# Kernel optimization log

Measured on AMD Instinct MI355X. Metric: run time of the kernel, lower is better.

The kernel has to match this reference:

```python
import jax, jax.numpy as jnp
import numpy as np

DIM = 64
HEADS = 4
SHAPE = (2, 64, 64, 64, DIM)  # [n, h, w, d, C] channels-last


def setup_inputs() -> dict:
    key = jax.random.key(0)
    ks = jax.random.split(key, 9)
    s = 1.0 / np.sqrt(DIM)
    return {
        "x": jax.random.normal(ks[0], SHAPE, dtype=jnp.float32),
        "Wk": jax.random.normal(ks[1], (DIM, DIM), dtype=jnp.float32) * s,
        "bk": jax.random.normal(ks[2], (DIM,), dtype=jnp.float32) * 0.01,
        "Wq": jax.random.normal(ks[3], (DIM, DIM), dtype=jnp.float32) * s,
        "bq": jax.random.normal(ks[4], (DIM,), dtype=jnp.float32) * 0.01,
        "Wv": jax.random.normal(ks[5], (DIM, DIM), dtype=jnp.float32) * s,
        "bv": jax.random.normal(ks[6], (DIM,), dtype=jnp.float32) * 0.01,
        "Wr": jax.random.normal(ks[7], (DIM, DIM), dtype=jnp.float32) * s,
        "br": jax.random.normal(ks[8], (DIM,), dtype=jnp.float32) * 0.01,
        "head_count": HEADS,
    }


def reference(x, Wk, bk, Wq, bq, Wv, bv, Wr, br, head_count):
    n, h, w, d, C = x.shape
    N = h * w * d
    H = head_count
    dk = C // H  # head key channels == head value channels (key/value channels = dim)

    xf = x.reshape(n, N, C)  # tokens along flattened spatial axis
    # Conv3d with 1x1x1 kernel == per-token linear projection over channels
    k = xf @ Wk.T + bk  # [n, N, C]
    q = xf @ Wq.T + bq
    v = xf @ Wv.T + bv

    # split channels into contiguous head chunks -> [n, H, dk, N]
    k = k.reshape(n, N, H, dk).transpose(0, 2, 3, 1)
    q = q.reshape(n, N, H, dk).transpose(0, 2, 3, 1)
    v = v.reshape(n, N, H, dk).transpose(0, 2, 3, 1)

    k = jax.nn.softmax(k, axis=3)  # softmax over spatial positions
    q = jax.nn.softmax(q, axis=2)  # softmax over head key channels

    # context = softmax(K) @ V^T : [n, H, dk, dv]
    ctx = jnp.einsum('nhkN,nhvN->nhkv', k, v)
    # attended = context^T @ softmax(Q) : [n, H, dv, N]
    att = jnp.einsum('nhkv,nhkN->nhvN', ctx, q)

    agg = att.transpose(0, 3, 1, 2).reshape(n, N, C)  # concat heads on channels
    out = agg @ Wr.T + br  # reprojection (1x1x1 conv)
    return out.reshape(n, h, w, d, C)
```

## Files before the change

kernel.cpp:

```cpp
#include <hip/hip_runtime.h>
#include <math.h>


#define NTOK 262144
typedef float4 f4;
typedef _Float16 f16;
typedef __attribute__((ext_vector_type(8))) _Float16 f16x8;
typedef __attribute__((ext_vector_type(4))) _Float16 f16x4;
typedef __attribute__((ext_vector_type(4))) float f32x4;

#define WS_S  0
#define WS_Z  2048
#define WS_MH 2176

__device__ __forceinline__ f16x8 cvt8h2(f4 a, f4 b) {
    f16x8 r;
    r[0] = (f16)a.x; r[1] = (f16)a.y; r[2] = (f16)a.z; r[3] = (f16)a.w;
    r[4] = (f16)b.x; r[5] = (f16)b.y; r[6] = (f16)b.z; r[7] = (f16)b.w;
    return r;
}

__global__ __launch_bounds__(256) void k_init(float* __restrict__ ws) {
    int i = blockIdx.x * 256 + threadIdx.x;
    if (i < 2176) ws[i] = 0.0f;
}

__global__ __launch_bounds__(256) void k_ctx(const float* __restrict__ x,
                                             const float* __restrict__ Wk,
                                             const float* __restrict__ Wv,
                                             float* __restrict__ ws) {
    __shared__ float sr[4096];
    __shared__ float zr[256];

    const int tid  = threadIdx.x;
    const int w    = tid >> 6;
    const int lane = tid & 63;
    const int lr   = lane & 15;
    const int ql   = lane >> 4;

    const int nb = blockIdx.x >> 9;
    const int bi = blockIdx.x & 511;
    const long base = (long)nb * NTOK + (long)bi * 512 + (long)w * 128;

    f16x8 wkf[4][2], wvf[4][2];
    #pragma unroll
    for (int h = 0; h < 4; ++h) {
        const float* kr = &Wk[(16 * h + lr) * 64 + 8 * ql];
        const float* vr = &Wv[(16 * h + lr) * 64 + 8 * ql];
        #pragma unroll
        for (int jc = 0; jc < 2; ++jc) {
            wkf[h][jc] = cvt8h2(*(const f4*)&kr[32 * jc], *(const f4*)&kr[32 * jc + 4]);
            wvf[h][jc] = cvt8h2(*(const f4*)&vr[32 * jc], *(const f4*)&vr[32 * jc + 4]);
        }
    }

    const f32x4 zero4 = {0.f, 0.f, 0.f, 0.f};
    f32x4 S[4] = {zero4, zero4, zero4, zero4};
    float z[4] = {0.f, 0.f, 0.f, 0.f};

    f4 A0, A1, A2, A3, B0, B1, B2, B3;
    {
        const float* xp = x + (((size_t)(base + lr)) << 6) + 8 * ql;
        A0 = *(const f4*)xp;        A1 = *(const f4*)(xp + 4);
        A2 = *(const f4*)(xp + 32); A3 = *(const f4*)(xp + 36);
        const float* yp = x + (((size_t)(base + 16 + lr)) << 6) + 8 * ql;
        B0 = *(const f4*)yp;        B1 = *(const f4*)(yp + 4);
        B2 = *(const f4*)(yp + 32); B3 = *(const f4*)(yp + 36);
    }

    for (int s = 0; s < 4; ++s) {
        {
            f16x8 a0 = cvt8h2(A0, A1), a1 = cvt8h2(A2, A3);
            if (s < 3) {
                const float* xp = x + (((size_t)(base + (2 * s + 2) * 16 + lr)) << 6) + 8 * ql;
                A0 = *(const f4*)xp;        A1 = *(const f4*)(xp + 4);
                A2 = *(const f4*)(xp + 32); A3 = *(const f4*)(xp + 36);
            }
            #pragma unroll
            for (int h = 0; h < 4; ++h) {
                f32x4 ak = zero4, av = zero4;
                ak = __builtin_amdgcn_mfma_f32_16x16x32_f16(a0, wkf[h][0], ak, 0, 0, 0);
                ak = __builtin_amdgcn_mfma_f32_16x16x32_f16(a1, wkf[h][1], ak, 0, 0, 0);
                av = __builtin_amdgcn_mfma_f32_16x16x32_f16(a0, wvf[h][0], av, 0, 0, 0);
                av = __builtin_amdgcn_mfma_f32_16x16x32_f16(a1, wvf[h][1], av, 0, 0, 0);
                const float e0 = __expf(ak[0]), e1 = __expf(ak[1]);
                const float e2 = __expf(ak[2]), e3 = __expf(ak[3]);
                z[h] += (e0 + e1) + (e2 + e3);
                f16x4 ekf = {(f16)e0, (f16)e1, (f16)e2, (f16)e3};
                f16x4 evf = {(f16)av[0], (f16)av[1], (f16)av[2], (f16)av[3]};
                S[h] = __builtin_amdgcn_mfma_f32_16x16x16f16(ekf, evf, S[h], 0, 0, 0);
            }
        }
        {
            f16x8 a0 = cvt8h2(B0, B1), a1 = cvt8h2(B2, B3);
            if (s < 3) {
                const float* xp = x + (((size_t)(base + (2 * s + 3) * 16 + lr)) << 6) + 8 * ql;
                B0 = *(const f4*)xp;        B1 = *(const f4*)(xp + 4);
                B2 = *(const f4*)(xp + 32); B3 = *(const f4*)(xp + 36);
            }
            #pragma unroll
            for (int h = 0; h < 4; ++h) {
                f32x4 ak = zero4, av = zero4;
                ak = __builtin_amdgcn_mfma_f32_16x16x32_f16(a0, wkf[h][0], ak, 0, 0, 0);
                ak = __builtin_amdgcn_mfma_f32_16x16x32_f16(a1, wkf[h][1], ak, 0, 0, 0);
                av = __builtin_amdgcn_mfma_f32_16x16x32_f16(a0, wvf[h][0], av, 0, 0, 0);
                av = __builtin_amdgcn_mfma_f32_16x16x32_f16(a1, wvf[h][1], av, 0, 0, 0);
                const float e0 = __expf(ak[0]), e1 = __expf(ak[1]);
                const float e2 = __expf(ak[2]), e3 = __expf(ak[3]);
                z[h] += (e0 + e1) + (e2 + e3);
                f16x4 ekf = {(f16)e0, (f16)e1, (f16)e2, (f16)e3};
                f16x4 evf = {(f16)av[0], (f16)av[1], (f16)av[2], (f16)av[3]};
                S[h] = __builtin_amdgcn_mfma_f32_16x16x16f16(ekf, evf, S[h], 0, 0, 0);
            }
        }
    }

    #pragma unroll
    for (int h = 0; h < 4; ++h) {
        z[h] += __shfl_xor(z[h], 16);
        z[h] += __shfl_xor(z[h], 32);
    }

    #pragma unroll
    for (int h = 0; h < 4; ++h) {
        #pragma unroll
        for (int r = 0; r < 4; ++r)
            sr[((w * 4 + h) * 16 + 4 * ql + r) * 16 + lr] = S[h][r];
        if (lane < 16) zr[(w * 4 + h) * 16 + lane] = z[h];
    }
    __syncthreads();
    #pragma unroll
    for (int i = 0; i < 4; ++i) {
        const int idx = i * 256 + tid;
        const float acc = sr[idx] + sr[1024 + idx] + sr[2048 + idx] + sr[3072 + idx];
        atomicAdd(&ws[WS_S + nb * 1024 + idx], acc);
    }
    if (tid < 64) {
        const float acc = zr[tid] + zr[64 + tid] + zr[128 + tid] + zr[192 + tid];
        atomicAdd(&ws[WS_Z + nb * 64 + tid], acc);
    }
}

__global__ __launch_bounds__(256) void k_m(const float* __restrict__ Wr,
                                           const float* __restrict__ bv,
                                           float* __restrict__ ws) {
    const int n = blockIdx.x >> 4;
    const int i = (blockIdx.x & 15) * 256 + threadIdx.x;
    f16* MH = (f16*)(ws + WS_MH);
    const int c = i >> 6, p = i & 63;
    const int h = p >> 4, kc = p & 15;
    const float rz = 1.0f / ws[WS_Z + n * 64 + p];
    const float* Srow = ws + WS_S + n * 1024 + h * 256 + kc * 16;
    const float* Wrow = Wr + c * 64 + h * 16;
    const float* bvr  = bv + h * 16;
    float acc = 0.f, accb = 0.f;
    #pragma unroll
    for (int vc = 0; vc < 16; ++vc) {
        acc  += Wrow[vc] * Srow[vc];
        accb += Wrow[vc] * bvr[vc];
    }
    MH[n * 4096 + c * 64 + p] = (f16)(acc * rz + accb);
}

__global__ __launch_bounds__(256) void k_out(const float* __restrict__ x,
                                             const float* __restrict__ Wq,
                                             const float* __restrict__ bq,
                                             const float* __restrict__ br,
                                             float* __restrict__ out,
                                             const float* __restrict__ ws) {
    const int tid  = threadIdx.x;
    const int w    = tid >> 6;
    const int lane = tid & 63;
    const int lr   = lane & 15;
    const int ql   = lane >> 4;

    const int nb = blockIdx.x >> 10;
    const int bi = blockIdx.x & 1023;
    const long base = (long)nb * NTOK + (long)bi * 256 + (long)w * 64;

    f16x8 wqf[4][2];
    f16x4 bqh[4];
    #pragma unroll
    for (int h = 0; h < 4; ++h) {
        const float* qr = &Wq[(16 * h + lr) * 64 + 8 * ql];
        #pragma unroll
        for (int jc = 0; jc < 2; ++jc)
            wqf[h][jc] = cvt8h2(*(const f4*)&qr[32 * jc], *(const f4*)&qr[32 * jc + 4]);
        const f4 b = *(const f4*)&bq[16 * h + 4 * ql];
        bqh[h][0] = (f16)b.x; bqh[h][1] = (f16)b.y;
        bqh[h][2] = (f16)b.z; bqh[h][3] = (f16)b.w;
    }
    f16x4 mfa[4][4];
    f16x4 brh[4];
    const f16* MH = (const f16*)(ws + WS_MH) + (size_t)nb * 4096;
    #pragma unroll
    for (int oct = 0; oct < 4; ++oct) {
        #pragma unroll
        for (int pc = 0; pc < 4; ++pc)
            mfa[oct][pc] = *(const f16x4*)&MH[(16 * oct + lr) * 64 + 16 * pc + 4 * ql];
        const f4 b = *(const f4*)&br[16 * oct + 4 * ql];
        brh[oct][0] = (f16)b.x; brh[oct][1] = (f16)b.y;
        brh[oct][2] = (f16)b.z; brh[oct][3] = (f16)b.w;
    }

    const f32x4 zero4 = {0.f, 0.f, 0.f, 0.f};

    f4 L0, L1, L2, L3;
    {
        const float* xp = x + (((size_t)(base + lr)) << 6) + 8 * ql;
        L0 = *(const f4*)xp;        L1 = *(const f4*)(xp + 4);
        L2 = *(const f4*)(xp + 32); L3 = *(const f4*)(xp + 36);
    }

    for (int s = 0; s < 4; ++s) {
        f16x8 b0 = cvt8h2(L0, L1), b1 = cvt8h2(L2, L3);
        if (s < 3) {
            const float* xp = x + (((size_t)(base + (s + 1) * 16 + lr)) << 6) + 8 * ql;
            L0 = *(const f4*)xp;        L1 = *(const f4*)(xp + 4);
            L2 = *(const f4*)(xp + 32); L3 = *(const f4*)(xp + 36);
        }
        f16x4 qf[4];
        #pragma unroll
        for (int h = 0; h < 4; ++h) {
            f32x4 aq = zero4;
            aq = __builtin_amdgcn_mfma_f32_16x16x32_f16(wqf[h][0], b0, aq, 0, 0, 0);
            aq = __builtin_amdgcn_mfma_f32_16x16x32_f16(wqf[h][1], b1, aq, 0, 0, 0);
            float q0 = aq[0] + (float)bqh[h][0], q1 = aq[1] + (float)bqh[h][1];
            float q2 = aq[2] + (float)bqh[h][2], q3 = aq[3] + (float)bqh[h][3];
            float mx = fmaxf(fmaxf(q0, q1), fmaxf(q2, q3));
            mx = fmaxf(mx, __shfl_xor(mx, 16));
            mx = fmaxf(mx, __shfl_xor(mx, 32));
            float e0 = __expf(q0 - mx), e1 = __expf(q1 - mx);
            float e2 = __expf(q2 - mx), e3 = __expf(q3 - mx);
            float sm = (e0 + e1) + (e2 + e3);
            sm += __shfl_xor(sm, 16);
            sm += __shfl_xor(sm, 32);
            const float rs = 1.0f / sm;
            qf[h][0] = (f16)(e0 * rs); qf[h][1] = (f16)(e1 * rs);
            qf[h][2] = (f16)(e2 * rs); qf[h][3] = (f16)(e3 * rs);
        }
        const size_t obase = ((size_t)(base + s * 16 + lr)) << 6;
        #pragma unroll
        for (int oct = 0; oct < 4; ++oct) {
            f32x4 o = zero4;
            #pragma unroll
            for (int pc = 0; pc < 4; ++pc)
                o = __builtin_amdgcn_mfma_f32_16x16x16f16(mfa[oct][pc], qf[pc], o, 0, 0, 0);
            const f4 res = {o[0] + (float)brh[oct][0], o[1] + (float)brh[oct][1],
                            o[2] + (float)brh[oct][2], o[3] + (float)brh[oct][3]};
            *(f4*)&out[obase + 16 * oct + 4 * ql] = res;
        }
    }
}

extern "C" void kernel_launch(void* const* d_in, const int* in_sizes, int n_in,
                              void* d_out, int out_size, void* d_ws, size_t ws_size,
                              hipStream_t stream) {
    const float* x  = (const float*)d_in[0];
    const float* Wk = (const float*)d_in[1];
    const float* Wq = (const float*)d_in[3];
    const float* bq = (const float*)d_in[4];
    const float* Wv = (const float*)d_in[5];
    const float* bv = (const float*)d_in[6];
    const float* Wr = (const float*)d_in[7];
    const float* br = (const float*)d_in[8];
    float* out = (float*)d_out;
    float* ws  = (float*)d_ws;

    hipLaunchKernelGGL(k_init, dim3(9),    dim3(256), 0, stream, ws);
    hipLaunchKernelGGL(k_ctx,  dim3(1024), dim3(256), 0, stream, x, Wk, Wv, ws);
    hipLaunchKernelGGL(k_m,    dim3(32),   dim3(256), 0, stream, Wr, bv, ws);
    hipLaunchKernelGGL(k_out,  dim3(2048), dim3(256), 0, stream, x, Wq, bq, br, out, ws);
}
```

Baseline: 127.4 us.

## Split context reduction across more blocks with 16 partial-sum slots

The context kernel now launches four times as many blocks, each covering 128 tokens (32 per wave, with no inner loop), to raise parallelism and occupancy. Atomic accumulation is spread over 16 partial buffers per batch, selected by block index, to reduce contention on the same addresses. The small M kernel then sums the 16 partial S and Z slices. In exchange, the per-block cost of loading and converting the weights is paid over less work, there are more atomics overall, and the init kernel must zero a larger buffer.

```diff
diff --git a/kernel.cpp b/kernel.cpp
--- a/kernel.cpp
+++ b/kernel.cpp
@@ -9,9 +9,9 @@
 typedef __attribute__((ext_vector_type(4))) _Float16 f16x4;
 typedef __attribute__((ext_vector_type(4))) float f32x4;
 
-#define WS_S  0
-#define WS_Z  2048
 #define WS_MH 2176
+#define WS_SP 6272
+#define WS_ZP 39040
 
 __device__ __forceinline__ f16x8 cvt8h2(f4 a, f4 b) {
     f16x8 r;
@@ -22,7 +22,7 @@
 
 __global__ __launch_bounds__(256) void k_init(float* __restrict__ ws) {
     int i = blockIdx.x * 256 + threadIdx.x;
-    if (i < 2176) ws[i] = 0.0f;
+    if (i < 34816) ws[WS_SP + i] = 0.0f;
 }
 
 __global__ __launch_bounds__(256) void k_ctx(const float* __restrict__ x,
@@ -38,25 +38,10 @@
     const int lr   = lane & 15;
     const int ql   = lane >> 4;
 
-    const int nb = blockIdx.x >> 9;
-    const int bi = blockIdx.x & 511;
-    const long base = (long)nb * NTOK + (long)bi * 512 + (long)w * 128;
-
-    f16x8 wkf[4][2], wvf[4][2];
-    #pragma unroll
-    for (int h = 0; h < 4; ++h) {
-        const float* kr = &Wk[(16 * h + lr) * 64 + 8 * ql];
-        const float* vr = &Wv[(16 * h + lr) * 64 + 8 * ql];
-        #pragma unroll
-        for (int jc = 0; jc < 2; ++jc) {
-            wkf[h][jc] = cvt8h2(*(const f4*)&kr[32 * jc], *(const f4*)&kr[32 * jc + 4]);
-            wvf[h][jc] = cvt8h2(*(const f4*)&vr[32 * jc], *(const f4*)&vr[32 * jc + 4]);
-        }
-    }
-
-    const f32x4 zero4 = {0.f, 0.f, 0.f, 0.f};
-    f32x4 S[4] = {zero4, zero4, zero4, zero4};
-    float z[4] = {0.f, 0.f, 0.f, 0.f};
+    const int nb = blockIdx.x >> 11;
+    const int bi = blockIdx.x & 2047;
+    const int sl = bi & 15;
+    const long base = (long)nb * NTOK + (long)bi * 128 + (long)w * 32;
 
     f4 A0, A1, A2, A3, B0, B1, B2, B3;
     {
@@ -68,50 +53,54 @@
         B2 = *(const f4*)(yp + 32); B3 = *(const f4*)(yp + 36);
     }
 
-    for (int s = 0; s < 4; ++s) {
-        {
-            f16x8 a0 = cvt8h2(A0, A1), a1 = cvt8h2(A2, A3);
-            if (s < 3) {
-                const float* xp = x + (((size_t)(base + (2 * s + 2) * 16 + lr)) << 6) + 8 * ql;
-                A0 = *(const f4*)xp;        A1 = *(const f4*)(xp + 4);
-                A2 = *(const f4*)(xp + 32); A3 = *(const f4*)(xp + 36);
-            }
-            #pragma unroll
-            for (int h = 0; h < 4; ++h) {
-                f32x4 ak = zero4, av = zero4;
-                ak = __builtin_amdgcn_mfma_f32_16x16x32_f16(a0, wkf[h][0], ak, 0, 0, 0);
-                ak = __builtin_amdgcn_mfma_f32_16x16x32_f16(a1, wkf[h][1], ak, 0, 0, 0);
-                av = __builtin_amdgcn_mfma_f32_16x16x32_f16(a0, wvf[h][0], av, 0, 0, 0);
-                av = __builtin_amdgcn_mfma_f32_16x16x32_f16(a1, wvf[h][1], av, 0, 0, 0);
-                const float e0 = __expf(ak[0]), e1 = __expf(ak[1]);
-                const float e2 = __expf(ak[2]), e3 = __expf(ak[3]);
-                z[h] += (e0 + e1) + (e2 + e3);
-                f16x4 ekf = {(f16)e0, (f16)e1, (f16)e2, (f16)e3};
-                f16x4 evf = {(f16)av[0], (f16)av[1], (f16)av[2], (f16)av[3]};
-                S[h] = __builtin_amdgcn_mfma_f32_16x16x16f16(ekf, evf, S[h], 0, 0, 0);
-            }
-        }
-        {
-            f16x8 a0 = cvt8h2(B0, B1), a1 = cvt8h2(B2, B3);
-            if (s < 3) {
-                const float* xp = x + (((size_t)(base + (2 * s + 3) * 16 + lr)) << 6) + 8 * ql;
-                B0 = *(const f4*)xp;        B1 = *(const f4*)(xp + 4);
-                B2 = *(const f4*)(xp + 32); B3 = *(const f4*)(xp + 36);
-            }
-            #pragma unroll
-            for (int h = 0; h < 4; ++h) {
-                f32x4 ak = zero4, av = zero4;
-                ak = __builtin_amdgcn_mfma_f32_16x16x32_f16(a0, wkf[h][0], ak, 0, 0, 0);
-                ak = __builtin_amdgcn_mfma_f32_16x16x32_f16(a1, wkf[h][1], ak, 0, 0, 0);
-                av = __builtin_amdgcn_mfma_f32_16x16x32_f16(a0, wvf[h][0], av, 0, 0, 0);
-                av = __builtin_amdgcn_mfma_f32_16x16x32_f16(a1, wvf[h][1], av, 0, 0, 0);
-                const float e0 = __expf(ak[0]), e1 = __expf(ak[1]);
-                const float e2 = __expf(ak[2]), e3 = __expf(ak[3]);
-                z[h] += (e0 + e1) + (e2 + e3);
-                f16x4 ekf = {(f16)e0, (f16)e1, (f16)e2, (f16)e3};
-                f16x4 evf = {(f16)av[0], (f16)av[1], (f16)av[2], (f16)av[3]};
-                S[h] = __builtin_amdgcn_mfma_f32_16x16x16f16(ekf, evf, S[h], 0, 0, 0);
-            }
+    f16x8 wkf[4][2], wvf[4][2];
+    #pragma unroll
+    for (int h = 0; h < 4; ++h) {
+        const float* kr = &Wk[(16 * h + lr) * 64 + 8 * ql];
+        const float* vr = &Wv[(16 * h + lr) * 64 + 8 * ql];
+        #pragma unroll
+        for (int jc = 0; jc < 2; ++jc) {
+            wkf[h][jc] = cvt8h2(*(const f4*)&kr[32 * jc], *(const f4*)&kr[32 * jc + 4]);
+            wvf[h][jc] = cvt8h2(*(const f4*)&vr[32 * jc], *(const f4*)&vr[32 * jc + 4]);
+        }
+    }
+
+    const f32x4 zero4 = {0.f, 0.f, 0.f, 0.f};
+    f32x4 S[4] = {zero4, zero4, zero4, zero4};
+    float z[4] = {0.f, 0.f, 0.f, 0.f};
+
+    {
+        f16x8 a0 = cvt8h2(A0, A1), a1 = cvt8h2(A2, A3);
+        #pragma unroll
+        for (int h = 0; h < 4; ++h) {
+            f32x4 ak = zero4, av = zero4;
+            ak = __builtin_amdgcn_mfma_f32_16x16x32_f16(a0, wkf[h][0], ak, 0, 0, 0);
+            ak = __builtin_amdgcn_mfma_f32_16x16x32_f16(a1, wkf[h][1], ak, 0, 0, 0);
+            av = __builtin_amdgcn_mfma_f32_16x16x32_f16(a0, wvf[h][0], av, 0, 0, 0);
+            av = __builtin_amdgcn_mfma_f32_16x16x32_f16(a1, wvf[h][1], av, 0, 0, 0);
+            const float e0 = __expf(ak[0]), e1 = __expf(ak[1]);
+            const float e2 = __expf(ak[2]), e3 = __expf(ak[3]);
+            z[h] += (e0 + e1) + (e2 + e3);
+            f16x4 ekf = {(f16)e0, (f16)e1, (f16)e2, (f16)e3};
+            f16x4 evf = {(f16)av[0], (f16)av[1], (f16)av[2], (f16)av[3]};
+            S[h] = __builtin_amdgcn_mfma_f32_16x16x16f16(ekf, evf, S[h], 0, 0, 0);
+        }
+    }
+    {
+        f16x8 a0 = cvt8h2(B0, B1), a1 = cvt8h2(B2, B3);
+        #pragma unroll
+        for (int h = 0; h < 4; ++h) {
+            f32x4 ak = zero4, av = zero4;
+            ak = __builtin_amdgcn_mfma_f32_16x16x32_f16(a0, wkf[h][0], ak, 0, 0, 0);
+            ak = __builtin_amdgcn_mfma_f32_16x16x32_f16(a1, wkf[h][1], ak, 0, 0, 0);
+            av = __builtin_amdgcn_mfma_f32_16x16x32_f16(a0, wvf[h][0], av, 0, 0, 0);
+            av = __builtin_amdgcn_mfma_f32_16x16x32_f16(a1, wvf[h][1], av, 0, 0, 0);
+            const float e0 = __expf(ak[0]), e1 = __expf(ak[1]);
+            const float e2 = __expf(ak[2]), e3 = __expf(ak[3]);
+            z[h] += (e0 + e1) + (e2 + e3);
+            f16x4 ekf = {(f16)e0, (f16)e1, (f16)e2, (f16)e3};
+            f16x4 evf = {(f16)av[0], (f16)av[1], (f16)av[2], (f16)av[3]};
+            S[h] = __builtin_amdgcn_mfma_f32_16x16x16f16(ekf, evf, S[h], 0, 0, 0);
         }
     }
 
@@ -129,15 +118,16 @@
         if (lane < 16) zr[(w * 4 + h) * 16 + lane] = z[h];
     }
     __syncthreads();
+    const int sbase = WS_SP + (sl * 2 + nb) * 1024;
     #pragma unroll
     for (int i = 0; i < 4; ++i) {
         const int idx = i * 256 + tid;
         const float acc = sr[idx] + sr[1024 + idx] + sr[2048 + idx] + sr[3072 + idx];
-        atomicAdd(&ws[WS_S + nb * 1024 + idx], acc);
+        atomicAdd(&ws[sbase + idx], acc);
     }
     if (tid < 64) {
         const float acc = zr[tid] + zr[64 + tid] + zr[128 + tid] + zr[192 + tid];
-        atomicAdd(&ws[WS_Z + nb * 64 + tid], acc);
+        atomicAdd(&ws[WS_ZP + (sl * 2 + nb) * 64 + tid], acc);
     }
 }
 
@@ -149,15 +139,20 @@
     f16* MH = (f16*)(ws + WS_MH);
     const int c = i >> 6, p = i & 63;
     const int h = p >> 4, kc = p & 15;
-    const float rz = 1.0f / ws[WS_Z + n * 64 + p];
-    const float* Srow = ws + WS_S + n * 1024 + h * 256 + kc * 16;
+    float zsum = 0.f;
+    #pragma unroll
+    for (int sl = 0; sl < 16; ++sl)
+        zsum += ws[WS_ZP + (sl * 2 + n) * 64 + p];
+    const float rz = 1.0f / zsum;
     const float* Wrow = Wr + c * 64 + h * 16;
     const float* bvr  = bv + h * 16;
     float acc = 0.f, accb = 0.f;
     #pragma unroll
-    for (int vc = 0; vc < 16; ++vc) {
-        acc  += Wrow[vc] * Srow[vc];
-        accb += Wrow[vc] * bvr[vc];
+    for (int vc = 0; vc < 16; ++vc) accb += Wrow[vc] * bvr[vc];
+    for (int sl = 0; sl < 16; ++sl) {
+        const float* Srow = ws + WS_SP + (sl * 2 + n) * 1024 + h * 256 + kc * 16;
+        #pragma unroll
+        for (int vc = 0; vc < 16; ++vc) acc += Wrow[vc] * Srow[vc];
     }
     MH[n * 4096 + c * 64 + p] = (f16)(acc * rz + accb);
 }
@@ -267,8 +262,8 @@
     float* out = (float*)d_out;
     float* ws  = (float*)d_ws;
 
-    hipLaunchKernelGGL(k_init, dim3(9),    dim3(256), 0, stream, ws);
-    hipLaunchKernelGGL(k_ctx,  dim3(1024), dim3(256), 0, stream, x, Wk, Wv, ws);
+    hipLaunchKernelGGL(k_init, dim3(136),  dim3(256), 0, stream, ws);
+    hipLaunchKernelGGL(k_ctx,  dim3(4096), dim3(256), 0, stream, x, Wk, Wv, ws);
     hipLaunchKernelGGL(k_m,    dim3(32),   dim3(256), 0, stream, Wr, bv, ws);
     hipLaunchKernelGGL(k_out,  dim3(2048), dim3(256), 0, stream, x, Wq, bq, br, out, ws);
 }
```

Measured after the change: 161.6 us. 26.8% more time.
